# Optimization experiments

Hardware: AMD Instinct MI355X
Metric: run time of the kernel (lower is better)

## Reference

```python
import jax, jax.numpy as jnp
import numpy as np

C = 64
N_H = 4
N_WIN = 16
WIN_L = 8   # compressor window length (overlapped)
WIN_S = 4   # compressor stride -> T//4 blocks


def _rms(x, eps=1e-6):
    return x * jax.lax.rsqrt(jnp.mean(x * x, axis=-1, keepdims=True) + eps)


def _rope(x, negate=False):
    # x: (..., L, D); rotate-half RoPE over positions 0..L-1
    L, D = x.shape[-2], x.shape[-1]
    half = D // 2
    inv_freq = 1.0 / (10000.0 ** (jnp.arange(half, dtype=x.dtype) / half))
    ang = jnp.arange(L, dtype=x.dtype)[:, None] * inv_freq  # (L, half)
    if negate:
        ang = -ang
    cos, sin = jnp.cos(ang), jnp.sin(ang)
    x1, x2 = x[..., :half], x[..., half:]
    return jnp.concatenate([x1 * cos - x2 * sin, x1 * sin + x2 * cos], axis=-1)


def _compress(H, W):
    # overlapped token compressor: windows of WIN_L, stride WIN_S, zero-pad tail
    B, T, d = H.shape
    Tc = T // WIN_S
    Hp = jnp.pad(H, ((0, 0), (0, WIN_L - WIN_S), (0, 0)))
    idx = WIN_S * jnp.arange(Tc)[:, None] + jnp.arange(WIN_L)[None, :]  # (Tc, WIN_L)
    win = Hp[:, idx]                       # (B, Tc, WIN_L, d)
    return win.reshape(B, Tc, WIN_L * d) @ W  # (B, Tc, out)


def setup_inputs() -> dict:
    key = jax.random.key(0)
    ks = jax.random.split(key, 11)
    B, T, d = 2, 2048, 256

    def w(k, shape, fan):
        return jax.random.normal(k, shape, jnp.float32) / np.float32(np.sqrt(fan))

    H = jax.random.normal(ks[0], (B, T, d), jnp.float32)
    return {
        'H': H,
        'Wc_comp': w(ks[1], (WIN_L * d, C), WIN_L * d),
        'Wc_idx': w(ks[2], (WIN_L * d, 32), WIN_L * d),
        'W_DQ': w(ks[3], (d, 64), d),
        'W_IUQ': w(ks[4], (64, 4 * 32), 64),
        'W_w': w(ks[5], (64, 4), 64),
        'W_Q': w(ks[6], (d, N_H * C), d),
        'W_KV': w(ks[7], (d, C), d),
        'g_q': jnp.ones((N_H, C), jnp.float32),
        'g_k': jnp.ones((C,), jnp.float32),
        'g_v': jnp.ones((C,), jnp.float32),
        'Wg0': w(ks[8], (2 * C, 64), 2 * C),
        'bg0': jnp.zeros((64,), jnp.float32),
        'Wg1': w(ks[9], (2 * C, 64), 2 * C),
        'bg1': jnp.zeros((64,), jnp.float32),
        'Wout': w(ks[10], (128, d), 128),
        'bout': jnp.zeros((d,), jnp.float32),
    }


def reference(H, Wc_comp, Wc_idx, W_DQ, W_IUQ, W_w, W_Q, W_KV,
              g_q, g_k, g_v, Wg0, bg0, Wg1, bg1, Wout, bout):
    B, T, d = H.shape
    Tc = T // 4
    k_top = min(8, Tc)

    # ---- lightning indexer ----
    H_dc = H @ W_DQ                                   # (B,T,64)
    Q_I = (H_dc @ W_IUQ).reshape(B, T, 4, 32)         # (B,T,4,32)
    W_Iw = (H_dc @ W_w)[..., None]                    # (B,T,4,1)
    K_I = _compress(H, Wc_idx)                        # (B,Tc,32)
    dot = jnp.einsum('bthc,bsc->bths', Q_I, K_I)      # (B,T,4,Tc)
    I_ts = (W_Iw * jax.nn.relu(dot)).sum(axis=2)      # (B,T,Tc)

    t = jnp.arange(T)[:, None]
    s = jnp.arange(Tc)[None, :]
    mask_I = jnp.where(4 * s <= t, 0.0, -jnp.inf)     # (T,Tc) causal over blocks
    _, topk_idx = jax.lax.top_k(I_ts + mask_I, k_top)  # (B,T,k)
    bI = jnp.arange(B)[:, None, None]
    tI = jnp.arange(T)[None, :, None]
    M_comp = jnp.full((B, T, Tc), -jnp.inf).at[bI, tI, topk_idx].set(0.0)

    # ---- compressed + sliding KV ----
    KV = jnp.concatenate([_compress(H, Wc_comp), H @ W_KV], axis=1)  # (B,Tc+T,C)

    Q = (H @ W_Q).reshape(B, T, N_H, C).transpose(0, 2, 1, 3)        # (B,nh,T,C)
    Q = _rms(Q) * g_q[None, :, None, :]
    K = _rms(KV) * g_k
    V = _rms(KV) * g_v
    Q = _rope(Q)
    K = _rope(K)
    V = _rope(V)

    S = jnp.einsum('bhtc,bsc->bhts', Q, K) / np.float32(np.sqrt(C))  # (B,nh,T,Tc+T)

    S_comp = S[..., :Tc] + M_comp[:, None]
    rel = t - jnp.arange(T)[None, :]
    mask_slide = jnp.where((rel >= 0) & (rel < N_WIN), 0.0, -jnp.inf)  # (T,T)
    S_slide = S[..., Tc:] + mask_slide

    P = jax.nn.softmax(jnp.concatenate([S_comp, S_slide], axis=-1), axis=-1)
    O = jnp.einsum('bhts,bsc->bhtc', P, V)            # (B,nh,T,C)
    O = _rope(O, negate=True)

    O0 = O[:, :2].transpose(0, 2, 1, 3).reshape(B, T, 2 * C)
    O1 = O[:, 2:].transpose(0, 2, 1, 3).reshape(B, T, 2 * C)
    p_all = jnp.concatenate([O0 @ Wg0 + bg0, O1 @ Wg1 + bg1], axis=-1)
    return p_all @ Wout + bout
```

## Files before the change

kernel.cpp:

```cpp
#include <hip/hip_runtime.h>
#include <hip/hip_bf16.h>
#include <math.h>

#define T_DIM 2048
#define B_DIM 2
#define D_DIM 256
#define TC 512
#define KV_LEN 2560

typedef __attribute__((ext_vector_type(8))) short bf16x8;
typedef __attribute__((ext_vector_type(4))) float f32x4;
typedef unsigned short ush;

__device__ __forceinline__ float wave_sum64(float v) {
#pragma unroll
    for (int off = 32; off > 0; off >>= 1) v += __shfl_xor(v, off, 64);
    return v;
}

__device__ __forceinline__ float rope_angle(int pos, int j) {
    float inv = powf(10000.0f, -(float)j * (1.0f / 32.0f));
    return (float)pos * inv;
}

__global__ __launch_bounds__(256) void k_prep(
    const float* __restrict__ H, const float* __restrict__ W_Q,
    const float* __restrict__ W_KV, const float* __restrict__ W_DQ,
    const float* __restrict__ W_IUQ, const float* __restrict__ W_w,
    const float* __restrict__ Wc_comp, const float* __restrict__ Wc_idx,
    const float* __restrict__ Wg0, const float* __restrict__ bg0,
    const float* __restrict__ Wg1, const float* __restrict__ bg1,
    const float* __restrict__ Wout, const float* __restrict__ bout,
    ush* __restrict__ Ap, ush* __restrict__ Ac,
    ush* __restrict__ Bp, ush* __restrict__ Bc,
    ush* __restrict__ Bo, float* __restrict__ biascomb)
{
    int gid = blockIdx.x * 256 + threadIdx.x;
    float vals[8];
    ush* dst;
    bool lo_part;

    if (gid < 262144) {
        int tile = gid >> 10;
        int c = (gid >> 6) & 15;
        int l = gid & 63;
        int bt = tile * 16 + (l & 15);
        int kb = (c & 7) * 32 + (l >> 4) * 8;
        const float* src = H + (size_t)bt * 256 + kb;
#pragma unroll
        for (int j = 0; j < 8; ++j) vals[j] = src[j];
        lo_part = (c >= 8);
        dst = Ap + (size_t)gid * 8;
    } else if (gid < 786432) {
        int g = gid - 262144;
        int tile = g >> 13;
        int c = (g >> 6) & 127;
        int l = g & 63;
        int m = tile * 16 + (l & 15);
        int s = m & 511;
        int b = m >> 9;
        int k2b = (c & 63) * 32 + (l >> 4) * 8;
        int r4 = 4 * s + (k2b >> 8);
        int col = k2b & 255;
        if (r4 < T_DIM) {
            const float* src = H + ((size_t)b * T_DIM + r4) * 256 + col;
#pragma unroll
            for (int j = 0; j < 8; ++j) vals[j] = src[j];
        } else {
#pragma unroll
            for (int j = 0; j < 8; ++j) vals[j] = 0.f;
        }
        lo_part = (c >= 64);
        dst = Ac + (size_t)g * 8;
    } else if (gid < 819200) {
        int g = gid - 786432;
        int tile = g >> 10;
        int c = (g >> 6) & 15;
        int l = g & 63;
        int n = tile * 16 + (l & 15);
        int kb = (c & 7) * 32 + (l >> 4) * 8;
#pragma unroll
        for (int j = 0; j < 8; ++j) {
            int k = kb + j;
            float w;
            if (n < 256)      w = W_Q[(size_t)k * 256 + n];
            else if (n < 320) w = W_KV[(size_t)k * 64 + (n - 256)];
            else if (n < 448) {
                w = 0.f;
                for (int i = 0; i < 64; ++i)
                    w = fmaf(W_DQ[(size_t)k * 64 + i], W_IUQ[(size_t)i * 128 + (n - 320)], w);
            } else if (n < 452) {
                w = 0.f;
                for (int i = 0; i < 64; ++i)
                    w = fmaf(W_DQ[(size_t)k * 64 + i], W_w[(size_t)i * 4 + (n - 448)], w);
            } else {
                w = 0.f;
            }
            vals[j] = w;
        }
        lo_part = (c >= 8);
        dst = Bp + (size_t)g * 8;
    } else if (gid < 868352) {
        int g = gid - 819200;
        int tile = g >> 13;
        int c = (g >> 6) & 127;
        int l = g & 63;
        int n = tile * 16 + (l & 15);
        int k2b = (c & 63) * 32 + (l >> 4) * 8;
#pragma unroll
        for (int j = 0; j < 8; ++j) {
            int k = k2b + j;
            vals[j] = (n < 64) ? Wc_comp[(size_t)k * 64 + n]
                               : Wc_idx[(size_t)k * 32 + (n - 64)];
        }
        lo_part = (c >= 64);
        dst = Bc + (size_t)g * 8;
    } else if (gid < 933888) {
        int g = gid - 868352;
        int k = g >> 8;
        int n = g & 255;
        float acc = 0.f;
        if (k < 128) {
            for (int i = 0; i < 64; ++i)
                acc = fmaf(Wg0[k * 64 + i], Wout[(size_t)i * 256 + n], acc);
        } else {
            for (int i = 0; i < 64; ++i)
                acc = fmaf(Wg1[(k - 128) * 64 + i], Wout[(size_t)(64 + i) * 256 + n], acc);
        }
        __hip_bfloat16 hb = __float2bfloat16(acc);
        float hif = __bfloat162float(hb);
        __hip_bfloat16 lb = __float2bfloat16(acc - hif);
        int tile = n >> 4;
        int chi = k >> 5;
        int lane2 = (n & 15) + 16 * ((k >> 3) & 3);
        int j = k & 7;
        Bo[(size_t)(tile * 16 + chi) * 512 + lane2 * 8 + j] = *(ush*)&hb;
        Bo[(size_t)(tile * 16 + chi + 8) * 512 + lane2 * 8 + j] = *(ush*)&lb;
        return;
    } else if (gid < 934144) {
        int n = gid - 933888;
        float acc = bout[n];
        for (int i = 0; i < 64; ++i) {
            acc = fmaf(bg0[i], Wout[(size_t)i * 256 + n], acc);
            acc = fmaf(bg1[i], Wout[(size_t)(64 + i) * 256 + n], acc);
        }
        biascomb[n] = acc;
        return;
    } else {
        return;
    }

    bf16x8 out8;
#pragma unroll
    for (int j = 0; j < 8; ++j) {
        float x = vals[j];
        __hip_bfloat16 hb = __float2bfloat16(x);
        if (!lo_part) {
            out8[j] = *(short*)&hb;
        } else {
            float hif = __bfloat162float(hb);
            __hip_bfloat16 lb = __float2bfloat16(x - hif);
            out8[j] = *(short*)&lb;
        }
    }
    *(bf16x8*)dst = out8;
}

__global__ __launch_bounds__(64) void k_mfma(
    const ush* __restrict__ Ap, const ush* __restrict__ Ac,
    const ush* __restrict__ Bp, const ush* __restrict__ Bc,
    const float* __restrict__ g_q, const float* __restrict__ g_k,
    const float* __restrict__ g_v,
    float* __restrict__ Pre, float* __restrict__ Prec_part,
    float* __restrict__ Qr, float* __restrict__ Kbuf, float* __restrict__ Vbuf)
{
    int lane = threadIdx.x;
    int mrow = lane & 15;
    int q = lane >> 4;

    if (blockIdx.x < 512) {
        int p = blockIdx.x;
        int m0 = (p >> 2) * 32;
        int nq = p & 3;
        int n0 = nq * 128;
        int at0 = (m0 >> 4) * 16;
        int bt0n = (n0 >> 4) * 16;

        f32x4 acc[2][8];
#pragma unroll
        for (int mt = 0; mt < 2; ++mt)
#pragma unroll
            for (int nt = 0; nt < 8; ++nt) acc[mt][nt] = (f32x4){0.f, 0.f, 0.f, 0.f};

        for (int c = 0; c < 8; ++c) {
            bf16x8 ahi[2], alo[2], bhi[8], blo[8];
#pragma unroll
            for (int mt = 0; mt < 2; ++mt) {
                ahi[mt] = *(const bf16x8*)(Ap + (size_t)((at0 + mt * 16) + c) * 512 + lane * 8);
                alo[mt] = *(const bf16x8*)(Ap + (size_t)((at0 + mt * 16) + 8 + c) * 512 + lane * 8);
            }
#pragma unroll
            for (int nt = 0; nt < 8; ++nt) {
                bhi[nt] = *(const bf16x8*)(Bp + (size_t)((bt0n + nt * 16) + c) * 512 + lane * 8);
                blo[nt] = *(const bf16x8*)(Bp + (size_t)((bt0n + nt * 16) + 8 + c) * 512 + lane * 8);
            }
#pragma unroll
            for (int mt = 0; mt < 2; ++mt)
#pragma unroll
                for (int nt = 0; nt < 8; ++nt) {
                    acc[mt][nt] = __builtin_amdgcn_mfma_f32_16x16x32_bf16(ahi[mt], bhi[nt], acc[mt][nt], 0, 0, 0);
                    acc[mt][nt] = __builtin_amdgcn_mfma_f32_16x16x32_bf16(ahi[mt], blo[nt], acc[mt][nt], 0, 0, 0);
                    acc[mt][nt] = __builtin_amdgcn_mfma_f32_16x16x32_bf16(alo[mt], bhi[nt], acc[mt][nt], 0, 0, 0);
                }
        }

        if (nq < 2) {
            int h0 = nq * 2, h1 = nq * 2 + 1;
#pragma unroll
            for (int mt = 0; mt < 2; ++mt)
#pragma unroll
                for (int reg = 0; reg < 4; ++reg) {
                    int bt = m0 + 16 * mt + 4 * q + reg;
                    int t = bt & 2047;
                    float ss0 = 0.f, ss1 = 0.f;
#pragma unroll
                    for (int k = 0; k < 4; ++k) {
                        float v0 = acc[mt][k][reg];
                        float v1 = acc[mt][4 + k][reg];
                        ss0 = fmaf(v0, v0, ss0);
                        ss1 = fmaf(v1, v1, ss1);
                    }
#pragma unroll
                    for (int off = 1; off <= 8; off <<= 1) {
                        ss0 += __shfl_xor(ss0, off, 64);
                        ss1 += __shfl_xor(ss1, off, 64);
                    }
                    float sc0 = rsqrtf(ss0 * (1.0f / 64.0f) + 1e-6f);
                    float sc1 = rsqrtf(ss1 * (1.0f / 64.0f) + 1e-6f);
#pragma unroll
                    for (int k = 0; k < 2; ++k) {
                        int jj = 16 * k + mrow;
                        float sa, ca;
                        sincosf(rope_angle(t, jj), &sa, &ca);
                        {
                            float x1 = acc[mt][k][reg] * sc0 * g_q[h0 * 64 + jj];
                            float x2 = acc[mt][k + 2][reg] * sc0 * g_q[h0 * 64 + 32 + jj];
                            Qr[(size_t)bt * 256 + h0 * 64 + jj] = fmaf(x1, ca, -x2 * sa);
                            Qr[(size_t)bt * 256 + h0 * 64 + 32 + jj] = fmaf(x1, sa, x2 * ca);
                        }
                        {
                            float x1 = acc[mt][4 + k][reg] * sc1 * g_q[h1 * 64 + jj];
                            float x2 = acc[mt][4 + k + 2][reg] * sc1 * g_q[h1 * 64 + 32 + jj];
                            Qr[(size_t)bt * 256 + h1 * 64 + jj] = fmaf(x1, ca, -x2 * sa);
                            Qr[(size_t)bt * 256 + h1 * 64 + 32 + jj] = fmaf(x1, sa, x2 * ca);
                        }
                    }
                }
        } else if (nq == 2) {
#pragma unroll
            for (int mt = 0; mt < 2; ++mt)
#pragma unroll
                for (int reg = 0; reg < 4; ++reg) {
                    int bt = m0 + 16 * mt + 4 * q + reg;
                    int b = bt >> 11;
                    int t = bt & 2047;
                    float ss = 0.f;
#pragma unroll
                    for (int k = 0; k < 4; ++k) {
                        float v = acc[mt][k][reg];
                        ss = fmaf(v, v, ss);
                    }
#pragma unroll
                    for (int off = 1; off <= 8; off <<= 1) ss += __shfl_xor(ss, off, 64);
                    float sc = rsqrtf(ss * (1.0f / 64.0f) + 1e-6f);
                    int pos = TC + t;
                    size_t base = ((size_t)b * KV_LEN + pos) * 64;
#pragma unroll
                    for (int k = 0; k < 2; ++k) {
                        int jj = 16 * k + mrow;
                        float sa, ca;
                        sincosf(rope_angle(pos, jj), &sa, &ca);
                        float k1 = acc[mt][k][reg] * sc * g_k[jj];
                        float k2 = acc[mt][k + 2][reg] * sc * g_k[32 + jj];
                        float v1 = acc[mt][k][reg] * sc * g_v[jj];
                        float v2 = acc[mt][k + 2][reg] * sc * g_v[32 + jj];
                        Kbuf[base + jj] = fmaf(k1, ca, -k2 * sa);
                        Kbuf[base + 32 + jj] = fmaf(k1, sa, k2 * ca);
                        Vbuf[base + jj] = fmaf(v1, ca, -v2 * sa);
                        Vbuf[base + 32 + jj] = fmaf(v1, sa, v2 * ca);
                    }
#pragma unroll
                    for (int nt = 4; nt < 8; ++nt)
                        Pre[(size_t)bt * 512 + n0 + 16 * nt + mrow] = acc[mt][nt][reg];
                }
        } else {
#pragma unroll
            for (int mt = 0; mt < 2; ++mt)
#pragma unroll
                for (int nt = 0; nt < 8; ++nt)
#pragma unroll
                    for (int reg = 0; reg < 4; ++reg)
                        Pre[(size_t)(m0 + 16 * mt + 4 * q + reg) * 512 + n0 + 16 * nt + mrow] =
                            acc[mt][nt][reg];
        }
    } else {
        int cb = blockIdx.x - 512;
        int m0 = (cb >> 2) * 32;
        int q4 = cb & 3;
        int at0 = (m0 >> 4) * 128;

        f32x4 acc[2][6];
#pragma unroll
        for (int mt = 0; mt < 2; ++mt)
#pragma unroll
            for (int nt = 0; nt < 6; ++nt) acc[mt][nt] = (f32x4){0.f, 0.f, 0.f, 0.f};

        for (int cl = 0; cl < 16; ++cl) {
            int c = q4 * 16 + cl;
            bf16x8 ahi[2], alo[2], bhi[6], blo[6];
#pragma unroll
            for (int mt = 0; mt < 2; ++mt) {
                ahi[mt] = *(const bf16x8*)(Ac + (size_t)((at0 + mt * 128) + c) * 512 + lane * 8);
                alo[mt] = *(const bf16x8*)(Ac + (size_t)((at0 + mt * 128) + 64 + c) * 512 + lane * 8);
            }
#pragma unroll
            for (int nt = 0; nt < 6; ++nt) {
                bhi[nt] = *(const bf16x8*)(Bc + (size_t)(nt * 128 + c) * 512 + lane * 8);
                blo[nt] = *(const bf16x8*)(Bc + (size_t)(nt * 128 + 64 + c) * 512 + lane * 8);
            }
#pragma unroll
            for (int mt = 0; mt < 2; ++mt)
#pragma unroll
                for (int nt = 0; nt < 6; ++nt) {
                    acc[mt][nt] = __builtin_amdgcn_mfma_f32_16x16x32_bf16(ahi[mt], bhi[nt], acc[mt][nt], 0, 0, 0);
                    acc[mt][nt] = __builtin_amdgcn_mfma_f32_16x16x32_bf16(ahi[mt], blo[nt], acc[mt][nt], 0, 0, 0);
                    acc[mt][nt] = __builtin_amdgcn_mfma_f32_16x16x32_bf16(alo[mt], bhi[nt], acc[mt][nt], 0, 0, 0);
                }
        }

        float* dst = Prec_part + (size_t)q4 * (1024 * 96);
#pragma unroll
        for (int mt = 0; mt < 2; ++mt)
#pragma unroll
            for (int nt = 0; nt < 6; ++nt)
#pragma unroll
                for (int reg = 0; reg < 4; ++reg)
                    dst[(size_t)(m0 + 16 * mt + 4 * q + reg) * 96 + 16 * nt + mrow] =
                        acc[mt][nt][reg];
    }
}

__global__ __launch_bounds__(256) void k_epi(
    const float* __restrict__ Prec_part,
    const float* __restrict__ g_k, const float* __restrict__ g_v,
    float* __restrict__ KIbuf, float* __restrict__ Kbuf, float* __restrict__ Vbuf)
{
    int tid = threadIdx.x;
    int wv = tid >> 6;
    int lane = tid & 63;
    int sg = blockIdx.x * 4 + wv;
    int b = sg >> 9;
    int s = sg & 511;

    const float* p0 = Prec_part + (size_t)sg * 96;
    float kvv = p0[lane] + p0[98304 + lane] + p0[2 * 98304 + lane] + p0[3 * 98304 + lane];

    float ss = wave_sum64(kvv * kvv);
    float sc = rsqrtf(ss * (1.0f / 64.0f) + 1e-6f);
    float kk = kvv * sc * g_k[lane];
    float vv = kvv * sc * g_v[lane];
    int j = lane & 31;
    float sa, ca;
    sincosf(rope_angle(s, j), &sa, &ca);
    float pk = __shfl_xor(kk, 32, 64);
    float pv = __shfl_xor(vv, 32, 64);
    float ko = (lane < 32) ? fmaf(kk, ca, -pk * sa) : fmaf(pk, sa, kk * ca);
    float vo = (lane < 32) ? fmaf(vv, ca, -pv * sa) : fmaf(pv, sa, vv * ca);
    size_t off = ((size_t)b * KV_LEN + s) * 64 + lane;
    Kbuf[off] = ko;
    Vbuf[off] = vo;

    if (lane < 32) {
        float a = p0[64 + lane] + p0[98304 + 64 + lane] +
                  p0[2 * 98304 + 64 + lane] + p0[3 * 98304 + 64 + lane];
        KIbuf[((size_t)b * TC + s) * 32 + lane] = a;
    }
}

__global__ __launch_bounds__(256) void k_score_topk(
    const float* __restrict__ Pre, const float* __restrict__ KIbuf,
    int* __restrict__ topk)
{
    int tid = threadIdx.x;
    int wv = tid >> 6;
    int lane = tid & 63;
    int bt0 = blockIdx.x * 4;
    int bt = bt0 + wv;
    int b = bt >> 11;
    int t = bt & 2047;

    __shared__ float sQ[4][128];
    __shared__ float sw[4][4];
    __shared__ float sKI[64 * 33];

    const float* pr = Pre + (size_t)bt * 512;
    sQ[wv][lane] = pr[320 + lane];
    sQ[wv][64 + lane] = pr[384 + lane];
    if (lane < 4) sw[wv][lane] = pr[448 + lane];

    const float* KIb = KIbuf + (size_t)b * TC * 32;
    int smax = t >> 2;
    int smax_blk = ((bt0 + 3) & 2047) >> 2;

    float vals[8];
#pragma unroll
    for (int r = 0; r < 8; ++r) vals[r] = -INFINITY;

    for (int r = 0; r < 8; ++r) {
        if (r * 64 > smax_blk) break;
        __syncthreads();
        for (int i = tid; i < 512; i += 256) {
            int row = i >> 3;
            int cseg = (i & 7) * 4;
            float4 v = *(const float4*)(KIb + (size_t)(r * 64 + row) * 32 + cseg);
            float* dstp = &sKI[row * 33 + cseg];
            dstp[0] = v.x; dstp[1] = v.y; dstp[2] = v.z; dstp[3] = v.w;
        }
        __syncthreads();

        int s = r * 64 + lane;
        if (s <= smax) {
            float dd0 = 0.f, dd1 = 0.f, dd2 = 0.f, dd3 = 0.f;
#pragma unroll
            for (int c = 0; c < 32; ++c) {
                float kv = sKI[lane * 33 + c];
                dd0 = fmaf(sQ[wv][c], kv, dd0);
                dd1 = fmaf(sQ[wv][32 + c], kv, dd1);
                dd2 = fmaf(sQ[wv][64 + c], kv, dd2);
                dd3 = fmaf(sQ[wv][96 + c], kv, dd3);
            }
            vals[r] = sw[wv][0] * fmaxf(dd0, 0.f) + sw[wv][1] * fmaxf(dd1, 0.f) +
                      sw[wv][2] * fmaxf(dd2, 0.f) + sw[wv][3] * fmaxf(dd3, 0.f);
        }
    }

    unsigned consumed = 0u;
    for (int k2 = 0; k2 < 8; ++k2) {
        float bv = -INFINITY;
        int bi = 0x7fffffff;
#pragma unroll
        for (int r = 0; r < 8; ++r) {
            if (!(consumed & (1u << r))) {
                int s = lane + 64 * r;
                float v = vals[r];
                if (v > bv || (v == bv && s < bi)) { bv = v; bi = s; }
            }
        }
#pragma unroll
        for (int off = 1; off < 64; off <<= 1) {
            float ov = __shfl_xor(bv, off, 64);
            int oi = __shfl_xor(bi, off, 64);
            if (ov > bv || (ov == bv && oi < bi)) { bv = ov; bi = oi; }
        }
        if ((bi & 63) == lane) consumed |= 1u << (bi >> 6);
        if (lane == 0) topk[(size_t)bt * 8 + k2] = bi;
    }
}

__global__ __launch_bounds__(1024) void k_attn(
    const float* __restrict__ Qr, const float* __restrict__ Kbuf,
    const float* __restrict__ Vbuf, const int* __restrict__ topk,
    float* __restrict__ Obuf)
{
    int tid = threadIdx.x;
    int lt = tid >> 8;
    int t256 = tid & 255;
    int h = t256 >> 6;
    int lane = tid & 63;
    int bt0 = blockIdx.x * 4;
    int bt = bt0 + lt;
    int b = bt >> 11;
    int t = bt & 2047;
    int t0 = bt0 & 2047;

    __shared__ float sKV[102 * 65];
    __shared__ float sQ[4][256];
    __shared__ int sPos[4][8];
    __shared__ float sP[4][4][24];

    sQ[lt][t256] = Qr[(size_t)bt * 256 + t256];
    if (t256 < 8) sPos[lt][t256] = topk[(size_t)bt * 8 + t256];
    __syncthreads();

    for (int i = tid; i < 1632; i += 1024) {
        int row = i >> 4;
        int seg = (i & 15) << 2;
        const float* srcbase;
        bool ok = true;
        if (row < 38) {
            int idx = (row < 19) ? row : row - 19;
            int sp = t0 - 15 + idx;
            ok = (sp >= 0);
            srcbase = ((row < 19) ? Kbuf : Vbuf) +
                      ((size_t)b * KV_LEN + TC + sp) * 64;
        } else {
            int r = row - 38;
            int ltt = r >> 4;
            int slot = r & 15;
            int pos = sPos[ltt][slot & 7];
            srcbase = ((slot < 8) ? Kbuf : Vbuf) +
                      ((size_t)b * KV_LEN + pos) * 64;
        }
        if (ok) {
            float4 v = *(const float4*)(srcbase + seg);
            float* d = &sKV[row * 65 + seg];
            d[0] = v.x; d[1] = v.y; d[2] = v.z; d[3] = v.w;
        }
    }
    __syncthreads();

    float scv = -INFINITY;
    if (lane < 24) {
        int krow;
        bool valid;
        if (lane < 8) { krow = 38 + lt * 16 + lane; valid = true; }
        else          { krow = lt + 23 - lane; valid = (t - (lane - 8) >= 0); }
        if (valid) {
            float dd = 0.f;
#pragma unroll
            for (int c = 0; c < 64; ++c)
                dd = fmaf(sQ[lt][h * 64 + c], sKV[krow * 65 + c], dd);
            scv = dd * 0.125f;
        }
    }
    float m = scv;
#pragma unroll
    for (int off = 1; off < 64; off <<= 1) m = fmaxf(m, __shfl_xor(m, off, 64));
    float p = expf(scv - m);
    if (scv == -INFINITY) p = 0.f;
    float l = p;
#pragma unroll
    for (int off = 1; off < 64; off <<= 1) l += __shfl_xor(l, off, 64);
    p /= l;
    if (lane < 24) sP[lt][h][lane] = p;

    float o = 0.f;
#pragma unroll
    for (int j2 = 0; j2 < 8; ++j2) {
        int vrow = 38 + lt * 16 + 8 + j2;
        o = fmaf(sP[lt][h][j2], sKV[vrow * 65 + lane], o);
    }
#pragma unroll
    for (int j2 = 8; j2 < 24; ++j2) {
        if (t - (j2 - 8) >= 0) {
            int vrow = 19 + (lt + 23 - j2);
            o = fmaf(sP[lt][h][j2], sKV[vrow * 65 + lane], o);
        }
    }

    int j = lane & 31;
    float sa, ca;
    sincosf(rope_angle(t, j), &sa, &ca);
    float prt = __shfl_xor(o, 32, 64);
    float oo = (lane < 32) ? fmaf(o, ca, prt * sa) : fmaf(-prt, sa, o * ca);
    Obuf[(size_t)bt * 256 + h * 64 + lane] = oo;
}

__global__ __launch_bounds__(64) void k_out(
    const float* __restrict__ Obuf, const ush* __restrict__ Bo,
    const float* __restrict__ biascomb, float* __restrict__ out)
{
    int lane = threadIdx.x;
    int mrow = lane & 15;
    int q = lane >> 4;
    int p = blockIdx.x;
    int m0 = (p >> 2) * 32;
    int n0 = (p & 3) * 64;
    int bt0n = (n0 >> 4) * 16;

    f32x4 acc[2][4];
#pragma unroll
    for (int mt = 0; mt < 2; ++mt)
#pragma unroll
        for (int nt = 0; nt < 4; ++nt) acc[mt][nt] = (f32x4){0.f, 0.f, 0.f, 0.f};

    for (int c = 0; c < 8; ++c) {
        bf16x8 ahi[2], alo[2], bhi[4], blo[4];
#pragma unroll
        for (int mt = 0; mt < 2; ++mt) {
            const float* src = Obuf + (size_t)(m0 + 16 * mt + mrow) * 256 + c * 32 + 8 * q;
            float4 x0 = *(const float4*)src;
            float4 x1 = *(const float4*)(src + 4);
            float xs[8] = {x0.x, x0.y, x0.z, x0.w, x1.x, x1.y, x1.z, x1.w};
#pragma unroll
            for (int j = 0; j < 8; ++j) {
                __hip_bfloat16 hb = __float2bfloat16(xs[j]);
                float hif = __bfloat162float(hb);
                __hip_bfloat16 lb = __float2bfloat16(xs[j] - hif);
                ahi[mt][j] = *(short*)&hb;
                alo[mt][j] = *(short*)&lb;
            }
        }
#pragma unroll
        for (int nt = 0; nt < 4; ++nt) {
            bhi[nt] = *(const bf16x8*)(Bo + (size_t)((bt0n + nt * 16) + c) * 512 + lane * 8);
            blo[nt] = *(const bf16x8*)(Bo + (size_t)((bt0n + nt * 16) + 8 + c) * 512 + lane * 8);
        }
#pragma unroll
        for (int mt = 0; mt < 2; ++mt)
#pragma unroll
            for (int nt = 0; nt < 4; ++nt) {
                acc[mt][nt] = __builtin_amdgcn_mfma_f32_16x16x32_bf16(ahi[mt], bhi[nt], acc[mt][nt], 0, 0, 0);
                acc[mt][nt] = __builtin_amdgcn_mfma_f32_16x16x32_bf16(ahi[mt], blo[nt], acc[mt][nt], 0, 0, 0);
                acc[mt][nt] = __builtin_amdgcn_mfma_f32_16x16x32_bf16(alo[mt], bhi[nt], acc[mt][nt], 0, 0, 0);
            }
    }

#pragma unroll
    for (int mt = 0; mt < 2; ++mt)
#pragma unroll
        for (int nt = 0; nt < 4; ++nt) {
            float bia = biascomb[n0 + 16 * nt + mrow];
#pragma unroll
            for (int reg = 0; reg < 4; ++reg)
                out[(size_t)(m0 + 16 * mt + 4 * q + reg) * 256 + n0 + 16 * nt + mrow] =
                    acc[mt][nt][reg] + bia;
        }
}

extern "C" void kernel_launch(void* const* d_in, const int* in_sizes, int n_in,
                              void* d_out, int out_size, void* d_ws, size_t ws_size,
                              hipStream_t stream) {
    const float* H       = (const float*)d_in[0];
    const float* Wc_comp = (const float*)d_in[1];
    const float* Wc_idx  = (const float*)d_in[2];
    const float* W_DQ    = (const float*)d_in[3];
    const float* W_IUQ   = (const float*)d_in[4];
    const float* W_w     = (const float*)d_in[5];
    const float* W_Q     = (const float*)d_in[6];
    const float* W_KV    = (const float*)d_in[7];
    const float* g_q     = (const float*)d_in[8];
    const float* g_k     = (const float*)d_in[9];
    const float* g_v     = (const float*)d_in[10];
    const float* Wg0     = (const float*)d_in[11];
    const float* bg0     = (const float*)d_in[12];
    const float* Wg1     = (const float*)d_in[13];
    const float* bg1     = (const float*)d_in[14];
    const float* Wout    = (const float*)d_in[15];
    const float* bout    = (const float*)d_in[16];

    float* ws = (float*)d_ws;
    float* Qr   = ws;
    float* KI   = ws + 1048576;
    float* Kb   = ws + 1081344;
    float* Vb   = ws + 1409024;
    float* Pre  = ws + 1736704;
    float* Prec = ws + 3833856;
    float* Obuf = ws + 4227072;
    int* topkb  = (int*)(ws + 5275648);
    ush* Ap = (ush*)(ws + 5308416);
    ush* Ac = (ush*)(ws + 6356992);
    ush* Bp = (ush*)(ws + 8454144);
    ush* Bc = (ush*)(ws + 8585216);
    ush* Bo = (ush*)(ws + 8781824);
    float* biascomb = ws + 8847360;

    float* outp = (float*)d_out;

    hipLaunchKernelGGL(k_prep, dim3(3649), dim3(256), 0, stream,
                       H, W_Q, W_KV, W_DQ, W_IUQ, W_w, Wc_comp, Wc_idx,
                       Wg0, bg0, Wg1, bg1, Wout, bout,
                       Ap, Ac, Bp, Bc, Bo, biascomb);
    hipLaunchKernelGGL(k_mfma, dim3(640), dim3(64), 0, stream,
                       Ap, Ac, Bp, Bc, g_q, g_k, g_v, Pre, Prec, Qr, Kb, Vb);
    hipLaunchKernelGGL(k_epi, dim3(256), dim3(256), 0, stream,
                       Prec, g_k, g_v, KI, Kb, Vb);
    hipLaunchKernelGGL(k_score_topk, dim3(1024), dim3(256), 0, stream,
                       Pre, KI, topkb);
    hipLaunchKernelGGL(k_attn, dim3(1024), dim3(1024), 0, stream,
                       Qr, Kb, Vb, topkb, Obuf);
    hipLaunchKernelGGL(k_out, dim3(512), dim3(64), 0, stream,
                       Obuf, Bo, biascomb, outp);
}
```

Baseline: 174.3 us.

## Read compressor windows directly from packed H instead of materialising Ac

Removes the separate packed bf16 hi/lo buffer for the overlapped compressor windows (Ac), which duplicated each H row twice. The compressor MFMA path now computes the window row for each lane and loads fragments straight from the already-packed H buffer (Ap), zeroing rows past the sequence end. This shrinks the prep kernel grid and avoids writing and rereading a large intermediate. In exchange the per-lane A loads become gathered addresses with more index arithmetic, which may be less coalesced.

```diff
diff --git a/kernel.cpp b/kernel.cpp
--- a/kernel.cpp
+++ b/kernel.cpp
@@ -31,8 +31,7 @@
     const float* __restrict__ Wg0, const float* __restrict__ bg0,
     const float* __restrict__ Wg1, const float* __restrict__ bg1,
     const float* __restrict__ Wout, const float* __restrict__ bout,
-    ush* __restrict__ Ap, ush* __restrict__ Ac,
-    ush* __restrict__ Bp, ush* __restrict__ Bc,
+    ush* __restrict__ Ap, ush* __restrict__ Bp, ush* __restrict__ Bc,
     ush* __restrict__ Bo, float* __restrict__ biascomb)
 {
     int gid = blockIdx.x * 256 + threadIdx.x;
@@ -51,29 +50,8 @@
         for (int j = 0; j < 8; ++j) vals[j] = src[j];
         lo_part = (c >= 8);
         dst = Ap + (size_t)gid * 8;
-    } else if (gid < 786432) {
+    } else if (gid < 294912) {
         int g = gid - 262144;
-        int tile = g >> 13;
-        int c = (g >> 6) & 127;
-        int l = g & 63;
-        int m = tile * 16 + (l & 15);
-        int s = m & 511;
-        int b = m >> 9;
-        int k2b = (c & 63) * 32 + (l >> 4) * 8;
-        int r4 = 4 * s + (k2b >> 8);
-        int col = k2b & 255;
-        if (r4 < T_DIM) {
-            const float* src = H + ((size_t)b * T_DIM + r4) * 256 + col;
-#pragma unroll
-            for (int j = 0; j < 8; ++j) vals[j] = src[j];
-        } else {
-#pragma unroll
-            for (int j = 0; j < 8; ++j) vals[j] = 0.f;
-        }
-        lo_part = (c >= 64);
-        dst = Ac + (size_t)g * 8;
-    } else if (gid < 819200) {
-        int g = gid - 786432;
         int tile = g >> 10;
         int c = (g >> 6) & 15;
         int l = g & 63;
@@ -100,8 +78,8 @@
         }
         lo_part = (c >= 8);
         dst = Bp + (size_t)g * 8;
-    } else if (gid < 868352) {
-        int g = gid - 819200;
+    } else if (gid < 344064) {
+        int g = gid - 294912;
         int tile = g >> 13;
         int c = (g >> 6) & 127;
         int l = g & 63;
@@ -115,8 +93,8 @@
         }
         lo_part = (c >= 64);
         dst = Bc + (size_t)g * 8;
-    } else if (gid < 933888) {
-        int g = gid - 868352;
+    } else if (gid < 409600) {
+        int g = gid - 344064;
         int k = g >> 8;
         int n = g & 255;
         float acc = 0.f;
@@ -137,8 +115,8 @@
         Bo[(size_t)(tile * 16 + chi) * 512 + lane2 * 8 + j] = *(ush*)&hb;
         Bo[(size_t)(tile * 16 + chi + 8) * 512 + lane2 * 8 + j] = *(ush*)&lb;
         return;
-    } else if (gid < 934144) {
-        int n = gid - 933888;
+    } else if (gid < 409856) {
+        int n = gid - 409600;
         float acc = bout[n];
         for (int i = 0; i < 64; ++i) {
             acc = fmaf(bg0[i], Wout[(size_t)i * 256 + n], acc);
@@ -167,8 +145,8 @@
 }
 
 __global__ __launch_bounds__(64) void k_mfma(
-    const ush* __restrict__ Ap, const ush* __restrict__ Ac,
-    const ush* __restrict__ Bp, const ush* __restrict__ Bc,
+    const ush* __restrict__ Ap, const ush* __restrict__ Bp,
+    const ush* __restrict__ Bc,
     const float* __restrict__ g_q, const float* __restrict__ g_k,
     const float* __restrict__ g_v,
     float* __restrict__ Pre, float* __restrict__ Prec_part,
@@ -307,7 +285,7 @@
         int cb = blockIdx.x - 512;
         int m0 = (cb >> 2) * 32;
         int q4 = cb & 3;
-        int at0 = (m0 >> 4) * 128;
+        int bb = m0 >> 9;
 
         f32x4 acc[2][6];
 #pragma unroll
@@ -316,17 +294,34 @@
             for (int nt = 0; nt < 6; ++nt) acc[mt][nt] = (f32x4){0.f, 0.f, 0.f, 0.f};
 
         for (int cl = 0; cl < 16; ++cl) {
-            int c = q4 * 16 + cl;
+            int cc = q4 * 16 + cl;
+            int k2b = cc * 32 + q * 8;
+            int row_off = k2b >> 8;
+            int kcb = k2b & 255;
+            int chA = kcb >> 5;
+            int lsub = (kcb >> 3) & 3;
+
             bf16x8 ahi[2], alo[2], bhi[6], blo[6];
 #pragma unroll
             for (int mt = 0; mt < 2; ++mt) {
-                ahi[mt] = *(const bf16x8*)(Ac + (size_t)((at0 + mt * 128) + c) * 512 + lane * 8);
-                alo[mt] = *(const bf16x8*)(Ac + (size_t)((at0 + mt * 128) + 64 + c) * 512 + lane * 8);
+                int s_loc = (m0 & 511) + 16 * mt + mrow;
+                int r_loc = 4 * s_loc + row_off;
+                int r_glob = bb * 2048 + r_loc;
+                int tileA = r_glob >> 4;
+                int laneA = (r_glob & 15) + 16 * lsub;
+                bf16x8 h8 = *(const bf16x8*)(Ap + (size_t)(tileA * 16 + chA) * 512 + laneA * 8);
+                bf16x8 l8 = *(const bf16x8*)(Ap + (size_t)(tileA * 16 + chA + 8) * 512 + laneA * 8);
+                if (r_loc >= T_DIM) {
+#pragma unroll
+                    for (int j = 0; j < 8; ++j) { h8[j] = 0; l8[j] = 0; }
+                }
+                ahi[mt] = h8;
+                alo[mt] = l8;
             }
 #pragma unroll
             for (int nt = 0; nt < 6; ++nt) {
-                bhi[nt] = *(const bf16x8*)(Bc + (size_t)(nt * 128 + c) * 512 + lane * 8);
-                blo[nt] = *(const bf16x8*)(Bc + (size_t)(nt * 128 + 64 + c) * 512 + lane * 8);
+                bhi[nt] = *(const bf16x8*)(Bc + (size_t)(nt * 128 + cc) * 512 + lane * 8);
+                blo[nt] = *(const bf16x8*)(Bc + (size_t)(nt * 128 + 64 + cc) * 512 + lane * 8);
             }
 #pragma unroll
             for (int mt = 0; mt < 2; ++mt)
@@ -659,7 +654,6 @@
     float* Obuf = ws + 4227072;
     int* topkb  = (int*)(ws + 5275648);
     ush* Ap = (ush*)(ws + 5308416);
-    ush* Ac = (ush*)(ws + 6356992);
     ush* Bp = (ush*)(ws + 8454144);
     ush* Bc = (ush*)(ws + 8585216);
     ush* Bo = (ush*)(ws + 8781824);
@@ -667,12 +661,12 @@
 
     float* outp = (float*)d_out;
 
-    hipLaunchKernelGGL(k_prep, dim3(3649), dim3(256), 0, stream,
+    hipLaunchKernelGGL(k_prep, dim3(1601), dim3(256), 0, stream,
                        H, W_Q, W_KV, W_DQ, W_IUQ, W_w, Wc_comp, Wc_idx,
                        Wg0, bg0, Wg1, bg1, Wout, bout,
-                       Ap, Ac, Bp, Bc, Bo, biascomb);
+                       Ap, Bp, Bc, Bo, biascomb);
     hipLaunchKernelGGL(k_mfma, dim3(640), dim3(64), 0, stream,
-                       Ap, Ac, Bp, Bc, g_q, g_k, g_v, Pre, Prec, Qr, Kb, Vb);
+                       Ap, Bp, Bc, g_q, g_k, g_v, Pre, Prec, Qr, Kb, Vb);
     hipLaunchKernelGGL(k_epi, dim3(256), dim3(256), 0, stream,
                        Prec, g_k, g_v, KI, Kb, Vb);
     hipLaunchKernelGGL(k_score_topk, dim3(1024), dim3(256), 0, stream,
```

Measured after the change: 176.8 us. Within noise of the previous version (+1.5%).
